# Kernel tuning notes

Hardware: AMD Instinct MI355X
Metric: run time of the kernel (lower is better)

The kernel has to match this reference:

```python
import jax, jax.numpy as jnp
import numpy as np

B, N, DIN, U, K, DEG = 64, 512, 256, 128, 2, 8
BN = B * N
E = BN * DEG
D4 = 4 * U
HEADS = 2


def setup_inputs() -> dict:
    key = jax.random.key(0)
    ks = jax.random.split(key, 24)
    rng = np.random.default_rng(0)
    # block-diagonal batched graph: each of B graphs has N nodes, N*DEG random edges
    src = rng.integers(0, N, size=(B, N * DEG))
    dst = rng.integers(0, N, size=(B, N * DEG))
    off = (np.arange(B) * N)[:, None]
    edge_index = jnp.asarray(np.stack([(src + off).reshape(-1), (dst + off).reshape(-1)]), dtype=jnp.int32)

    def w(k, shape, fan):
        return (jax.random.normal(k, shape, dtype=jnp.float32) / np.sqrt(fan)).astype(jnp.float32)

    gin = (DIN + U) * (K + 1)  # gconv concatenates K+1 hop features of concat([x, h])
    inp = dict(
        x_od=jax.random.normal(ks[0], (BN, DIN), dtype=jnp.float32),
        history=jax.random.normal(ks[1], (BN, DIN), dtype=jnp.float32),
        yesterday=jax.random.normal(ks[2], (BN, DIN), dtype=jnp.float32),
        edge_index=edge_index,
        edge_weight=jax.random.uniform(ks[3], (E,), dtype=jnp.float32),
        W_ru_f=w(ks[4], (gin, 2 * U), gin), b_ru_f=jnp.zeros((2 * U,), jnp.float32),
        W_c_f=w(ks[5], (gin, U), gin), b_c_f=jnp.zeros((U,), jnp.float32),
        W_ru_l=w(ks[6], (gin, 2 * U), gin), b_ru_l=jnp.zeros((2 * U,), jnp.float32),
        W_c_l=w(ks[7], (gin, U), gin), b_c_l=jnp.zeros((U,), jnp.float32),
        W_ru_s=w(ks[8], (gin, 2 * U), gin), b_ru_s=jnp.zeros((2 * U,), jnp.float32),
        W_c_s=w(ks[9], (gin, U), gin), b_c_s=jnp.zeros((U,), jnp.float32),
        W_hd=w(ks[10], (D4, 2 * U), 2 * U), b_hd=jnp.zeros((D4,), jnp.float32),
        W_in=w(ks[11], (3 * D4, D4), D4), b_in=jnp.zeros((3 * D4,), jnp.float32),
        W_out=w(ks[12], (D4, D4), D4), b_out=jnp.zeros((D4,), jnp.float32),
        W_gate=w(ks[13], (U, D4), D4), b_gate=jnp.zeros((U,), jnp.float32),
    )
    return inp


def _gconv(x, src, dst, ew, W, b):
    # K-hop mean-normalized graph convolution over the batched edge list
    num = x.shape[0]
    deg = jnp.maximum(jax.ops.segment_sum(ew, dst, num_segments=num), 1.0)[:, None]
    feats = [x]
    h = x
    for _ in range(K):
        h = jax.ops.segment_sum(h[src] * ew[:, None], dst, num_segments=num) / deg
        feats.append(h)
    return jnp.concatenate(feats, axis=-1) @ W + b


def _ggru(x, h, src, dst, ew, W_ru, b_ru, W_c, b_c):
    ru = jax.nn.sigmoid(_gconv(jnp.concatenate([x, h], -1), src, dst, ew, W_ru, b_ru))
    r, u = jnp.split(ru, 2, axis=-1)
    c = jnp.tanh(_gconv(jnp.concatenate([x, r * h], -1), src, dst, ew, W_c, b_c))
    return u * h + (1.0 - u) * c


def _pos_enc(seq_len, d):
    pos = jnp.arange(seq_len, dtype=jnp.float32)[:, None]
    div = jnp.exp(jnp.arange(0, d, 2, dtype=jnp.float32) * (-jnp.log(10000.0) / d))
    pe = jnp.zeros((seq_len, d), jnp.float32)
    pe = pe.at[:, 0::2].set(jnp.sin(pos * div)).at[:, 1::2].set(jnp.cos(pos * div))
    return pe  # (seq_len, d)


def reference(x_od, history, yesterday, edge_index, edge_weight,
              W_ru_f, b_ru_f, W_c_f, b_c_f,
              W_ru_l, b_ru_l, W_c_l, b_c_l,
              W_ru_s, b_ru_s, W_c_s, b_c_s,
              W_hd, b_hd, W_in, b_in, W_out, b_out, W_gate, b_gate):
    src, dst = edge_index[0], edge_index[1]
    ew = edge_weight
    h0 = jnp.zeros((BN, U), jnp.float32)
    hf = _ggru(x_od, h0, src, dst, ew, W_ru_f, b_ru_f, W_c_f, b_c_f)      # finished branch
    hl = _ggru(history, h0, src, dst, ew, W_ru_l, b_ru_l, W_c_l, b_c_l)  # long-history branch
    hs = _ggru(yesterday, h0, src, dst, ew, W_ru_s, b_ru_s, W_c_s, b_c_s)  # short-history branch
    # hidden fusion: raw view(-1, 2U, N) as in the torch source
    fusion = jnp.concatenate([hs, hl], axis=-1).reshape(B, 2 * U, N)
    uh = jnp.einsum('oc,bcn->bon', W_hd, fusion) + b_hd[:, None]  # (B, 4U, N)
    uh = uh + _pos_enc(B, D4)[:, :, None]                          # pos-enc over batch dim, as in source
    x = uh.transpose(2, 0, 1)                                      # (N, B, 4U): seq=N, batch=B
    # multi-head self-attention (torch MultiheadAttention semantics)
    qkv = x @ W_in.T + b_in
    q, k_, v = jnp.split(qkv, 3, axis=-1)
    hd = D4 // HEADS
    qh = q.reshape(N, B, HEADS, hd)
    kh = k_.reshape(N, B, HEADS, hd)
    vh = v.reshape(N, B, HEADS, hd)
    scores = jnp.einsum('sbhd,tbhd->bhst', qh, kh) / jnp.sqrt(jnp.float32(hd))
    attn = jax.nn.softmax(scores, axis=-1)
    ctx = jnp.einsum('bhst,tbhd->sbhd', attn, vh).reshape(N, B, D4)
    attn_out = ctx @ W_out.T + b_out                               # (N, B, 4U)
    gated = jnp.einsum('oc,bcn->bon', W_gate, attn_out.transpose(1, 2, 0)) + b_gate[:, None]  # (B, U, N)
    attn_flat = gated.transpose(0, 2, 1).reshape(BN, U)
    # (enc_first_out==finished_hidden, long_hidden, short_hidden, gated attention)
    return jnp.stack([hf, hl, hs, attn_flat])
```

## Files before the change

### kernel.cpp

```cpp
#include <hip/hip_runtime.h>
#include <hip/hip_bf16.h>
#include <math.h>


#define DEV __device__ __forceinline__

typedef __attribute__((ext_vector_type(4))) float  f32x4;
typedef __attribute__((ext_vector_type(4))) float  fvec4;
typedef __attribute__((ext_vector_type(8))) short  bf16x8;
typedef __attribute__((ext_vector_type(4))) unsigned short u16x4;

constexpr int BN_ = 32768;
constexpr int E_  = 262144;
constexpr long OUTSEC = 4194304;
constexpr long ZSZE = 25165824;

DEV unsigned short f2bf(float f){
  union { float f; unsigned u; } v; v.f = f;
  unsigned r = (v.u + 0x7FFFu + ((v.u >> 16) & 1u)) >> 16;
  return (unsigned short)r;
}
DEV float b2f(unsigned short h){
  union { unsigned u; float f; } v; v.u = ((unsigned)h) << 16;
  return v.f;
}

__global__ __launch_bounds__(256) void histdeg_kernel(const int* __restrict__ ei,
    const float* __restrict__ ew, unsigned* __restrict__ cnt, float* __restrict__ deg){
  int e = blockIdx.x*256 + threadIdx.x;
  int d = ei[E_ + e];
  atomicAdd(&cnt[d], 1u);
  atomicAdd(&deg[d], ew[e]);
}

__global__ __launch_bounds__(1024) void scan_kernel(const unsigned* __restrict__ cnt,
                                                    unsigned* __restrict__ rowptr){
  __shared__ unsigned sm[1024];
  __shared__ unsigned carry;
  int tid = threadIdx.x;
  if (tid == 0) carry = 0;
  __syncthreads();
  for (int base = 0; base < BN_; base += 1024){
    unsigned v = cnt[base + tid];
    sm[tid] = v;
    __syncthreads();
    for (int off = 1; off < 1024; off <<= 1){
      unsigned t = (tid >= off) ? sm[tid - off] : 0u;
      __syncthreads();
      sm[tid] += t;
      __syncthreads();
    }
    rowptr[base + tid] = carry + sm[tid] - v;
    __syncthreads();
    if (tid == 1023) carry += sm[1023];
    __syncthreads();
  }
  if (tid == 0) rowptr[BN_] = carry;
}

__global__ __launch_bounds__(256) void scatter_kernel(const int* __restrict__ ei,
    const float* __restrict__ ew, const unsigned* __restrict__ rowptr,
    unsigned* __restrict__ curs, unsigned* __restrict__ csrc, float* __restrict__ csrw){
  int e = blockIdx.x*256 + threadIdx.x;
  int d = ei[E_ + e];
  unsigned pos = atomicAdd(&curs[d], 1u);
  unsigned idx = rowptr[d] + pos;
  csrc[idx] = (unsigned)ei[e];
  csrw[idx] = ew[e];
}

template<int SRC>
__global__ __launch_bounds__(256) void prop3_kernel(const float* __restrict__ x0,
    const float* __restrict__ x1, const float* __restrict__ x2,
    unsigned short* __restrict__ zcat,
    const unsigned* __restrict__ rowptr, const unsigned* __restrict__ csrc,
    const float* __restrict__ csrw, const float* __restrict__ deg){
  int node = blockIdx.x*4 + (threadIdx.x >> 6);
  int l = threadIdx.x & 63;
  int z = blockIdx.z;
  const float* xf = (z == 0) ? x0 : (z == 1) ? x1 : x2;
  const unsigned short* zin = zcat + z*ZSZE + 256;
  unsigned short* zout = zcat + z*ZSZE + (SRC == 0 ? 256 : 512);
  unsigned b0 = rowptr[node], b1 = rowptr[node + 1];
  float a0 = 0.f, a1 = 0.f, a2 = 0.f, a3 = 0.f;
  for (unsigned e = b0; e < b1; ++e){
    int s = csrc[e]; float w = csrw[e];
    if constexpr (SRC == 0){
      fvec4 v = *(const fvec4*)(xf + (long)s*256 + l*4);
      a0 += w*v[0]; a1 += w*v[1]; a2 += w*v[2]; a3 += w*v[3];
    } else {
      u16x4 v = *(const u16x4*)(zin + (long)s*768 + l*4);
      a0 += w*b2f(v[0]); a1 += w*b2f(v[1]); a2 += w*b2f(v[2]); a3 += w*b2f(v[3]);
    }
  }
  float dg = deg[node]; dg = dg > 1.f ? dg : 1.f;
  float inv = 1.f / dg;
  u16x4 o = { f2bf(a0*inv), f2bf(a1*inv), f2bf(a2*inv), f2bf(a3*inv) };
  *(u16x4*)(zout + (long)node*768 + l*4) = o;
}

__global__ __launch_bounds__(256) void convx3_kernel(const float* __restrict__ x0,
    const float* __restrict__ x1, const float* __restrict__ x2,
    unsigned short* __restrict__ zcat){
  int id = blockIdx.x*256 + threadIdx.x;
  int z = blockIdx.z;
  const float* xf = (z == 0) ? x0 : (z == 1) ? x1 : x2;
  fvec4 v = ((const fvec4*)xf)[id];
  int m = id >> 6, c4 = id & 63;
  u16x4 o = { f2bf(v[0]), f2bf(v[1]), f2bf(v[2]), f2bf(v[3]) };
  *(u16x4*)(zcat + z*ZSZE + (long)m*768 + c4*4) = o;
}

__global__ __launch_bounds__(256) void cvt_f2b_kernel(const float* __restrict__ s,
                                                      unsigned short* __restrict__ d, int n){
  int i = blockIdx.x*256 + threadIdx.x;
  if (i < n) d[i] = f2bf(s[i]);
}

__global__ __launch_bounds__(256) void tcvt_kernel(const float* __restrict__ s,
    unsigned short* __restrict__ d, int lgC, int R){
  int id = blockIdx.x*256 + threadIdx.x;
  int r = id >> lgC, c = id & ((1 << lgC) - 1);
  d[(long)c*R + r] = f2bf(s[id]);
}

__global__ __launch_bounds__(256) void weff3_kernel(
    const float* __restrict__ Wru0, const float* __restrict__ Wru1, const float* __restrict__ Wru2,
    const float* __restrict__ bru0, const float* __restrict__ bru1, const float* __restrict__ bru2,
    const float* __restrict__ Wc0,  const float* __restrict__ Wc1,  const float* __restrict__ Wc2,
    const float* __restrict__ bc0,  const float* __restrict__ bc1,  const float* __restrict__ bc2,
    unsigned short* __restrict__ Weff, float* __restrict__ beff){
  int z = blockIdx.y;
  const float* Wru = (z == 0) ? Wru0 : (z == 1) ? Wru1 : Wru2;
  const float* bru = (z == 0) ? bru0 : (z == 1) ? bru1 : bru2;
  const float* Wc  = (z == 0) ? Wc0  : (z == 1) ? Wc1  : Wc2;
  const float* bc  = (z == 0) ? bc0  : (z == 1) ? bc1  : bc2;
  int id = blockIdx.x*256 + threadIdx.x;
  int n = id / 768, k = id % 768;
  int row = (k >> 8)*384 + (k & 255);
  int j = n >> 1;
  float w = ((n & 1) == 0) ? Wru[(long)row*256 + 128 + j] : Wc[(long)row*128 + j];
  Weff[(long)z*196608 + (long)n*768 + k] = f2bf(w);
  if (k == 0) beff[z*256 + n] = ((n & 1) == 0) ? bru[128 + j] : bc[j];
}

__global__ __launch_bounds__(256) void pe_kernel(const float* __restrict__ bhd,
                                                 float* __restrict__ PET4){
  int id = blockIdx.x*256 + threadIdx.x;
  int b = id >> 9, o = id & 511;
  float j2 = (float)(o & ~1);
  float ang = (float)b * expf(-j2 * (9.210340371976184f / 512.f));
  float v = ((o & 1) ? cosf(ang) : sinf(ang)) + bhd[o];
  PET4[(o >> 2)*256 + b*4 + (o & 3)] = v;
}

__global__ __launch_bounds__(256) void peq2_kernel(const float* __restrict__ Win,
    const float* __restrict__ bin, const float* __restrict__ PET4, float* __restrict__ peq2){
  int j = blockIdx.x*4 + (threadIdx.x >> 6);
  int l = threadIdx.x & 63;
  float acc = 0.f;
  for (int o4 = 0; o4 < 128; ++o4){
    fvec4 wv = *(const fvec4*)(Win + (long)j*512 + o4*4);
    fvec4 pv = *(const fvec4*)(PET4 + o4*256 + l*4);
    acc += wv[0]*pv[0] + wv[1]*pv[1] + wv[2]*pv[2] + wv[3]*pv[3];
  }
  peq2[(long)l*1536 + j] = bin[j] + acc;
}

__global__ __launch_bounds__(128) void beq_kernel(const float* __restrict__ Wgt,
    const float* __restrict__ bout, const float* __restrict__ bgate, float* __restrict__ beq){
  int g = threadIdx.x;
  float s = bgate[g];
  for (int c = 0; c < 512; ++c) s += Wgt[(long)g*512 + c] * bout[c];
  beq[g] = s;
}

template<int MODE, int EPI>
__global__ __launch_bounds__(256) void gemm_bt(
    const unsigned short* __restrict__ A, const unsigned short* __restrict__ Bt,
    float* __restrict__ Cf, unsigned short* __restrict__ Cb,
    int Ktot, int lda, int ldb, int ldc,
    long sA, long sB, long sC, int g0,
    const float* __restrict__ bias, const float* __restrict__ pe, float scale)
{
  __shared__ unsigned short As[2][8192];
  __shared__ unsigned short Bs[2][8192];
  const int tid = threadIdx.x;
  long aOff, bOff, cOff;
  if constexpr (MODE == 0 || MODE == 3){
    aOff = blockIdx.z * sA; bOff = blockIdx.z * sB; cOff = blockIdx.z * sC;
  } else if constexpr (MODE == 1){
    int g = g0 + blockIdx.z;
    long base = (long)(g >> 1)*1536 + (long)(g & 1)*256;
    aOff = base; bOff = base + 512; cOff = (long)blockIdx.z * 262144;
  } else {
    int g = g0 + blockIdx.z;
    aOff = (long)blockIdx.z * 262144;
    bOff = (long)g * 131072;
    cOff = (long)g * 256;
  }
  const int bm = blockIdx.y * 128, bn = blockIdx.x * 128;
  const int w = tid >> 6, l = tid & 63;
  const int wr = w >> 1, wc = w & 1;

  const unsigned short* aB[4];
  const unsigned short* bB[4];
  #pragma unroll
  for (int i = 0; i < 4; ++i){
    int c = tid + i*256;
    int row = c >> 3, gg = c & 7;
    aB[i] = A  + aOff + (long)(bm + row)*lda + gg*8;
    bB[i] = Bt + bOff + (long)(bn + row)*ldb + gg*8;
  }

  f32x4 acc[4][4] = {};

  auto stage = [&](int p, int kt){
    #pragma unroll
    for (int i = 0; i < 4; ++i){
      __builtin_amdgcn_global_load_lds(
        (const __attribute__((address_space(1))) unsigned int*)(aB[i] + kt),
        (__attribute__((address_space(3))) unsigned int*)&As[p][(i*256 + w*64)*8], 16, 0, 0);
      __builtin_amdgcn_global_load_lds(
        (const __attribute__((address_space(1))) unsigned int*)(bB[i] + kt),
        (__attribute__((address_space(3))) unsigned int*)&Bs[p][(i*256 + w*64)*8], 16, 0, 0);
    }
  };
  auto compute = [&](int p){
    #pragma unroll
    for (int ks = 0; ks < 2; ++ks){
      bf16x8 aF[4], bF[4];
      #pragma unroll
      for (int mi = 0; mi < 4; ++mi)
        aF[mi] = *(const bf16x8*)(&As[p][(wr*64 + mi*16 + (l & 15))*64 + ks*32 + (l >> 4)*8]);
      #pragma unroll
      for (int ni = 0; ni < 4; ++ni)
        bF[ni] = *(const bf16x8*)(&Bs[p][(wc*64 + ni*16 + (l & 15))*64 + ks*32 + (l >> 4)*8]);
      #pragma unroll
      for (int mi = 0; mi < 4; ++mi)
        #pragma unroll
        for (int ni = 0; ni < 4; ++ni)
          acc[mi][ni] = __builtin_amdgcn_mfma_f32_16x16x32_bf16(aF[mi], bF[ni], acc[mi][ni], 0, 0, 0);
    }
  };

  const int nt = Ktot >> 6;
  stage(0, 0);
  __syncthreads();
  for (int t = 0; t < nt - 1; ++t){
    stage((t + 1) & 1, (t + 1) << 6);
    compute(t & 1);
    __syncthreads();
  }
  compute((nt - 1) & 1);

  #pragma unroll
  for (int mi = 0; mi < 4; ++mi){
    #pragma unroll
    for (int ni = 0; ni < 4; ++ni){
      int col = bn + wc*64 + ni*16 + (l & 15);
      int row0 = bm + wr*64 + mi*16 + ((l >> 4) << 2);
      #pragma unroll
      for (int j = 0; j < 4; ++j){
        int row = row0 + j;
        float v = acc[mi][ni][j] * scale;
        if (bias){
          if constexpr (MODE == 3) v += bias[(int)blockIdx.z*256 + col];
          else v += bias[col];
        }
        if constexpr (EPI == 5) v += pe[((row & 63) * 1536) + col];
        if constexpr (EPI == 0){
          Cf[cOff + (long)row*ldc + col] = v;
        } else if constexpr (EPI == 4){
          long orow = (long)(row & 63)*512 + (row >> 6);
          Cf[orow*ldc + col] = v;
        } else if constexpr (EPI == 7){
          float other = __shfl_xor(v, 1);
          if (!(l & 1)){
            float uu = 1.f / (1.f + expf(-v));
            Cf[cOff + (long)row*ldc + (col >> 1)] = (1.f - uu) * tanhf(other);
          }
        } else {
          Cb[cOff + (long)row*ldc + col] = f2bf(v);
        }
      }
    }
  }
}

__global__ __launch_bounds__(256) void afus_kernel(const float* __restrict__ out,
                                                   unsigned short* __restrict__ Afus){
  __shared__ float sm[64][132];
  int cq = blockIdx.x, a = blockIdx.y, b = blockIdx.z;
  int tid = threadIdx.x;
  #pragma unroll
  for (int half = 0; half < 2; ++half){
    const float* sec = out + (half ? 1 : 2)*OUTSEC;
    int cl = tid >> 2, r0 = (tid & 3)*4;
    long srow = ((long)b*512 + 2*(cq*64 + cl) + a)*128;
    #pragma unroll
    for (int it = 0; it < 8; ++it){
      int r = r0 + it*16;
      fvec4 v = *(const fvec4*)(sec + srow + r);
      *(fvec4*)&sm[cl][r] = v;
    }
    __syncthreads();
    int r = tid >> 1;
    int c0 = (tid & 1)*32;
    long mrow = ((long)a*256 + half*128 + r)*64 + b;
    unsigned short* dst = Afus + mrow*256 + cq*64 + c0;
    #pragma unroll
    for (int jj = 0; jj < 8; ++jj){
      int c = c0 + jj*4;
      u16x4 o = { f2bf(sm[c][r]), f2bf(sm[c+1][r]), f2bf(sm[c+2][r]), f2bf(sm[c+3][r]) };
      *(u16x4*)(dst + jj*4) = o;
    }
    __syncthreads();
  }
}

__global__ __launch_bounds__(256) void vt_kernel(const unsigned short* __restrict__ qkv,
                                                 unsigned short* __restrict__ vT){
  int g = blockIdx.y; int b = g >> 1, h = g & 1;
  int tt = blockIdx.x & 7, dt = blockIdx.x >> 3;
  __shared__ unsigned short sm[64][65];
  int lrow = threadIdx.x >> 6, lcol = threadIdx.x & 63;
  const unsigned short* src = qkv + (long)b*1536 + 1024 + (long)h*256 + dt*64;
  #pragma unroll
  for (int i = 0; i < 16; ++i){
    int t = tt*64 + lrow + i*4;
    sm[lrow + i*4][lcol] = src[(long)t*98304 + lcol];
  }
  __syncthreads();
  unsigned short* dstp = vT + (long)g*131072 + (long)(dt*64)*512 + tt*64;
  #pragma unroll
  for (int i = 0; i < 16; ++i){
    int d = lrow + i*4;
    dstp[(long)d*512 + lcol] = sm[lcol][d];
  }
}

__global__ __launch_bounds__(256) void smax_kernel(unsigned short* __restrict__ S){
  long row = (long)blockIdx.x*4 + (threadIdx.x >> 6);
  int l = threadIdx.x & 63;
  unsigned short* p = S + row*512 + l*8;
  bf16x8 v = *(const bf16x8*)p;
  float f[8];
  #pragma unroll
  for (int j = 0; j < 8; ++j) f[j] = b2f((unsigned short)v[j]);
  float m = f[0];
  #pragma unroll
  for (int j = 1; j < 8; ++j) m = fmaxf(m, f[j]);
  #pragma unroll
  for (int off = 32; off; off >>= 1) m = fmaxf(m, __shfl_xor(m, off));
  float s = 0.f;
  #pragma unroll
  for (int j = 0; j < 8; ++j){ f[j] = expf(f[j] - m); s += f[j]; }
  #pragma unroll
  for (int off = 32; off; off >>= 1) s += __shfl_xor(s, off);
  float inv = 1.f / s;
  bf16x8 o;
  #pragma unroll
  for (int j = 0; j < 8; ++j) o[j] = (short)f2bf(f[j]*inv);
  *(bf16x8*)p = o;
}

extern "C" void kernel_launch(void* const* d_in, const int* in_sizes, int n_in,
                              void* d_out, int out_size, void* d_ws, size_t ws_size,
                              hipStream_t stream)
{
  (void)in_sizes; (void)n_in; (void)out_size;
  constexpr long MB = 1l << 20;
  if (ws_size < 200*MB) return;

  const float* x0 = (const float*)d_in[0];
  const float* x1 = (const float*)d_in[1];
  const float* x2 = (const float*)d_in[2];
  const int*   ei = (const int*)d_in[3];
  const float* ew = (const float*)d_in[4];
  const float* Whd  = (const float*)d_in[17]; const float* bhd   = (const float*)d_in[18];
  const float* Win  = (const float*)d_in[19]; const float* bin   = (const float*)d_in[20];
  const float* Wout = (const float*)d_in[21]; const float* bout  = (const float*)d_in[22];
  const float* Wgt  = (const float*)d_in[23]; const float* bgate = (const float*)d_in[24];
  float* out = (float*)d_out;
  char* ws = (char*)d_ws;

  float*    deg    = (float*)(ws + 0);
  unsigned* cnt    = (unsigned*)(ws + 131072);
  unsigned* rowptr = (unsigned*)(ws + 262144);
  unsigned* curs   = (unsigned*)(ws + 524288);
  unsigned* csrc   = (unsigned*)(ws + 786432);
  float*    csrw   = (float*)(ws + 1835008);
  unsigned short* Weff = (unsigned short*)(ws + 2883584);
  float*    beff   = (float*)(ws + 4063232);
  float*    beq    = (float*)(ws + 4194304);
  unsigned short* WIN   = (unsigned short*)(ws + 4456448);
  unsigned short* WGTB  = (unsigned short*)(ws + 6029312);
  unsigned short* WHDT  = (unsigned short*)(ws + 6160384);
  unsigned short* WOUTT = (unsigned short*)(ws + 6422528);
  unsigned short* Wq2t  = (unsigned short*)(ws + 6946816);
  unsigned short* Weqt  = (unsigned short*)(ws + 7733248);
  float*    PET4   = (float*)(ws + 7864320);
  float*    PEQ2   = (float*)(ws + 7995392);
  unsigned short* ZCAT3 = (unsigned short*)(ws + 40*MB);
  unsigned short* AFUS  = (unsigned short*)(ws + 8*MB);
  unsigned short* QKV   = (unsigned short*)(ws + 40*MB);
  unsigned short* VT    = (unsigned short*)(ws + 8*MB);
  unsigned short* SCOREB= (unsigned short*)(ws + 136*MB);
  unsigned short* CTX   = (unsigned short*)(ws + 40*MB);

  hipMemsetAsync(deg,  0, 131072, stream);
  hipMemsetAsync(cnt,  0, 131072, stream);
  hipMemsetAsync(curs, 0, 131072, stream);
  histdeg_kernel<<<1024, 256, 0, stream>>>(ei, ew, cnt, deg);
  scan_kernel<<<1, 1024, 0, stream>>>(cnt, rowptr);
  scatter_kernel<<<1024, 256, 0, stream>>>(ei, ew, rowptr, curs, csrc, csrw);

  weff3_kernel<<<dim3(768,3), 256, 0, stream>>>(
      (const float*)d_in[5], (const float*)d_in[9],  (const float*)d_in[13],
      (const float*)d_in[6], (const float*)d_in[10], (const float*)d_in[14],
      (const float*)d_in[7], (const float*)d_in[11], (const float*)d_in[15],
      (const float*)d_in[8], (const float*)d_in[12], (const float*)d_in[16],
      Weff, beff);
  cvt_f2b_kernel<<<3072, 256, 0, stream>>>(Win, WIN,  786432);
  cvt_f2b_kernel<<<256,  256, 0, stream>>>(Wgt, WGTB, 65536);
  tcvt_kernel<<<512,  256, 0, stream>>>(Whd,  WHDT,  8, 512);
  tcvt_kernel<<<1024, 256, 0, stream>>>(Wout, WOUTT, 9, 512);
  pe_kernel<<<128, 256, 0, stream>>>(bhd, PET4);

  gemm_bt<0,2><<<dim3(2,12,1), 256, 0, stream>>>(WIN, WHDT, nullptr, Wq2t,
      512, 512, 512, 256, 0,0,0, 0, nullptr, nullptr, 1.0f);
  gemm_bt<0,2><<<dim3(4,1,1), 256, 0, stream>>>(WGTB, WOUTT, nullptr, Weqt,
      512, 512, 512, 512, 0,0,0, 0, nullptr, nullptr, 1.0f);
  peq2_kernel<<<384, 256, 0, stream>>>(Win, bin, PET4, PEQ2);
  beq_kernel<<<1, 128, 0, stream>>>(Wgt, bout, bgate, beq);

  convx3_kernel<<<dim3(8192,1,3), 256, 0, stream>>>(x0, x1, x2, ZCAT3);
  prop3_kernel<0><<<dim3(8192,1,3), 256, 0, stream>>>(x0, x1, x2, ZCAT3,
                                                      rowptr, csrc, csrw, deg);
  prop3_kernel<1><<<dim3(8192,1,3), 256, 0, stream>>>(x0, x1, x2, ZCAT3,
                                                      rowptr, csrc, csrw, deg);
  gemm_bt<3,7><<<dim3(2,256,3), 256, 0, stream>>>(ZCAT3, Weff, out, nullptr,
      768, 768, 768, 128, ZSZE, 196608, OUTSEC, 0, beff, nullptr, 1.0f);

  afus_kernel<<<dim3(4,2,64), 256, 0, stream>>>(out, AFUS);
  gemm_bt<0,5><<<dim3(12,256,1), 256, 0, stream>>>(AFUS, Wq2t, nullptr, QKV,
      256, 256, 256, 1536, 0,0,0, 0, nullptr, PEQ2, 1.0f);
  vt_kernel<<<dim3(32,128), 256, 0, stream>>>(QKV, VT);

  gemm_bt<1,2><<<dim3(4,4,128), 256, 0, stream>>>(QKV, QKV, nullptr, SCOREB,
      256, 98304, 98304, 512, 0,0,0, 0, nullptr, nullptr, 0.0625f);
  smax_kernel<<<16384, 256, 0, stream>>>(SCOREB);
  gemm_bt<2,2><<<dim3(2,4,128), 256, 0, stream>>>(SCOREB, VT, nullptr, CTX,
      512, 512, 512, 32768, 0,0,0, 0, nullptr, nullptr, 1.0f);

  gemm_bt<0,4><<<dim3(1,256,1), 256, 0, stream>>>(CTX, Weqt, out + 3*OUTSEC, nullptr,
      512, 512, 512, 128, 0,0,0, 0, beq, nullptr, 1.0f);
}
```

Before: 1.010 ms.

## Load B fragments directly from global, single-buffer swizzled A tile in LDS

```diff
diff --git a/kernel.cpp b/kernel.cpp
--- a/kernel.cpp
+++ b/kernel.cpp
@@ -183,8 +183,7 @@
     long sA, long sB, long sC, int g0,
     const float* __restrict__ bias, const float* __restrict__ pe, float scale)
 {
-  __shared__ unsigned short As[2][8192];
-  __shared__ unsigned short Bs[2][8192];
+  __shared__ unsigned short As[128*64];
   const int tid = threadIdx.x;
   long aOff, bOff, cOff;
   if constexpr (MODE == 0 || MODE == 3){
@@ -204,56 +203,49 @@
   const int wr = w >> 1, wc = w & 1;
 
   const unsigned short* aB[4];
-  const unsigned short* bB[4];
   #pragma unroll
   for (int i = 0; i < 4; ++i){
     int c = tid + i*256;
     int row = c >> 3, gg = c & 7;
-    aB[i] = A  + aOff + (long)(bm + row)*lda + gg*8;
-    bB[i] = Bt + bOff + (long)(bn + row)*ldb + gg*8;
-  }
+    int ggs = gg ^ (row & 7);
+    aB[i] = A + aOff + (long)(bm + row)*lda + ggs*8;
+  }
+  const unsigned short* bR[4];
+  #pragma unroll
+  for (int ni = 0; ni < 4; ++ni)
+    bR[ni] = Bt + bOff + (long)(bn + wc*64 + ni*16 + (l & 15))*ldb + (l >> 4)*8;
+  int aRow[4];
+  #pragma unroll
+  for (int mi = 0; mi < 4; ++mi) aRow[mi] = wr*64 + mi*16 + (l & 15);
 
   f32x4 acc[4][4] = {};
-
-  auto stage = [&](int p, int kt){
+  for (int kt = 0; kt < Ktot; kt += 64){
     #pragma unroll
-    for (int i = 0; i < 4; ++i){
+    for (int i = 0; i < 4; ++i)
       __builtin_amdgcn_global_load_lds(
         (const __attribute__((address_space(1))) unsigned int*)(aB[i] + kt),
-        (__attribute__((address_space(3))) unsigned int*)&As[p][(i*256 + w*64)*8], 16, 0, 0);
-      __builtin_amdgcn_global_load_lds(
-        (const __attribute__((address_space(1))) unsigned int*)(bB[i] + kt),
-        (__attribute__((address_space(3))) unsigned int*)&Bs[p][(i*256 + w*64)*8], 16, 0, 0);
-    }
-  };
-  auto compute = [&](int p){
+        (__attribute__((address_space(3))) unsigned int*)&As[(i*256 + w*64)*8], 16, 0, 0);
+    __syncthreads();
     #pragma unroll
     for (int ks = 0; ks < 2; ++ks){
       bf16x8 aF[4], bF[4];
       #pragma unroll
-      for (int mi = 0; mi < 4; ++mi)
-        aF[mi] = *(const bf16x8*)(&As[p][(wr*64 + mi*16 + (l & 15))*64 + ks*32 + (l >> 4)*8]);
+      for (int ni = 0; ni < 4; ++ni)
+        bF[ni] = *(const bf16x8*)(bR[ni] + kt + ks*32);
       #pragma unroll
-      for (int ni = 0; ni < 4; ++ni)
-        bF[ni] = *(const bf16x8*)(&Bs[p][(wc*64 + ni*16 + (l & 15))*64 + ks*32 + (l >> 4)*8]);
+      for (int mi = 0; mi < 4; ++mi){
+        int r = aRow[mi];
+        int gr = (ks*4 + (l >> 4)) ^ (r & 7);
+        aF[mi] = *(const bf16x8*)(&As[r*64 + gr*8]);
+      }
       #pragma unroll
       for (int mi = 0; mi < 4; ++mi)
         #pragma unroll
         for (int ni = 0; ni < 4; ++ni)
           acc[mi][ni] = __builtin_amdgcn_mfma_f32_16x16x32_bf16(aF[mi], bF[ni], acc[mi][ni], 0, 0, 0);
     }
-  };
-
-  const int nt = Ktot >> 6;
-  stage(0, 0);
-  __syncthreads();
-  for (int t = 0; t < nt - 1; ++t){
-    stage((t + 1) & 1, (t + 1) << 6);
-    compute(t & 1);
-    __syncthreads();
-  }
-  compute((nt - 1) & 1);
-
+    __syncthreads();
+  }
   #pragma unroll
   for (int mi = 0; mi < 4; ++mi){
     #pragma unroll
```

After: 1.033 ms. +2.3%, slower.
